# Performance work log

Hardware: AMD Instinct MI355X
Metric: run time of the kernel (lower is better)

The kernel has to match this reference:

```python
import jax, jax.numpy as jnp
import numpy as np
import math

C = 512
EPS = 1e-5


def _ln(x, g, b):
    m = jnp.mean(x, axis=-1, keepdims=True)
    v = jnp.var(x, axis=-1, keepdims=True)
    return (x - m) * jax.lax.rsqrt(v + EPS) * g + b


def _attn(x, w_qkv, w_out):
    # x: (..., L, C); attention over axis -2 (axial)
    qkv = jnp.einsum('...lc,dc->...ld', x, w_qkv)          # (..., L, 3C)
    qkv = qkv.reshape(*qkv.shape[:-1], C, 3)               # interleaved split as in torch reshape(*shape,3)
    q, k, v = qkv[..., 0], qkv[..., 1], qkv[..., 2]
    scale = 1.0 / math.sqrt(C)
    logits = jnp.einsum('...qc,...kc->...qk', q, k) * scale
    p = jax.nn.softmax(logits, axis=-1)
    ctx = jnp.einsum('...qk,...kc->...qc', p, v)
    return jnp.einsum('...lc,dc->...ld', ctx, w_out)


def setup_inputs() -> dict:
    key = jax.random.key(0)
    ks = jax.random.split(key, 16)
    s = 0.02
    inp = {
        'x': jax.random.normal(ks[0], (8, C, 48, 192), jnp.float32),
        'w_qkv1': jax.random.normal(ks[1], (3 * C, C), jnp.float32) * s,
        'w_out1': jax.random.normal(ks[2], (C, C), jnp.float32) * s,
        'w_qkv2': jax.random.normal(ks[3], (3 * C, C), jnp.float32) * s,
        'w_out2': jax.random.normal(ks[4], (C, C), jnp.float32) * s,
        'g1': jnp.ones((C,), jnp.float32), 'b1': jnp.zeros((C,), jnp.float32),
        'g2': jnp.ones((C,), jnp.float32), 'b2': jnp.zeros((C,), jnp.float32),
        'g3': jnp.ones((C,), jnp.float32), 'b3': jnp.zeros((C,), jnp.float32),
        'w_fc1': jax.random.normal(ks[5], (4 * C, C), jnp.float32) * s,
        'b_fc1': jnp.zeros((4 * C,), jnp.float32),
        'w_fc2': jax.random.normal(ks[6], (C, 4 * C), jnp.float32) * s,
        'b_fc2': jnp.zeros((C,), jnp.float32),
    }
    return inp


def reference(x, w_qkv1, w_out1, w_qkv2, w_out2, g1, b1, g2, b2, g3, b3,
              w_fc1, b_fc1, w_fc2, b_fc2):
    # x: (B, C, H, W) -> (B, W, H, C)
    x = jnp.transpose(x, (0, 3, 2, 1))
    x = x + _attn(_ln(x, g1, b1), w_qkv1, w_out1)          # attention along H
    # (B, W, H, C) -> (B, H, W, C)
    x = jnp.transpose(x, (0, 2, 1, 3))
    x = x + _attn(_ln(x, g2, b2), w_qkv2, w_out2)          # attention along W
    h = _ln(x, g3, b3)
    h = jax.nn.relu(jnp.einsum('bhwc,dc->bhwd', h, w_fc1) + b_fc1)
    x = x + jnp.einsum('bhwd,cd->bhwc', h, w_fc2) + b_fc2
    # (B, H, W, C) -> (B, C, H, W)
    return jnp.transpose(x, (0, 3, 1, 2))
```

## Files before the change

### kernel.cpp

```cpp
#include <hip/hip_runtime.h>

typedef unsigned short u16;
typedef __attribute__((ext_vector_type(8))) short short8;
typedef __attribute__((ext_vector_type(8))) __bf16 bf16x8;
typedef __attribute__((ext_vector_type(4))) float f32x4;

#define DEV __device__ __forceinline__

DEV u16 f2bf(float f){ unsigned u = __float_as_uint(f); return (u16)((u + 0x7fffu + ((u>>16)&1u)) >> 16); }
DEV float bf2f(u16 h){ return __uint_as_float(((unsigned)h)<<16); }

DEV f32x4 mfma_bf16(short8 a, short8 b, f32x4 c){
  return __builtin_amdgcn_mfma_f32_16x16x32_bf16(
      __builtin_bit_cast(bf16x8, a), __builtin_bit_cast(bf16x8, b), c, 0, 0, 0);
}

DEV void gl2lds16(const u16* g, u16* s){
  __builtin_amdgcn_global_load_lds(
      (__attribute__((address_space(1))) void*)(g),
      (__attribute__((address_space(3))) void*)(s), 16, 0, 0);
}

#define BB 8
#define HH 48
#define WW 192
#define CC 512
#define NTOK (BB*HH*WW)

__global__ void k_permqkv(const float* __restrict__ w, u16* __restrict__ o){
  int i = blockIdx.x*256 + threadIdx.x;
  int n = i >> 9, kk = i & 511;
  int src = 3*(n & 511) + (n >> 9);
  o[i] = f2bf(w[src*512 + kk]);
}
__global__ void k_conv(const float* __restrict__ w, u16* __restrict__ o, int nelem){
  int i = blockIdx.x*256 + threadIdx.x;
  if (i < nelem) o[i] = f2bf(w[i]);
}

__global__ void k_tin(const float* __restrict__ x, float* __restrict__ xr){
  __shared__ float T[32][33];
  int bh = blockIdx.x / 96, rem = blockIdx.x % 96;
  int c0 = (rem/6)*32, w0 = (rem%6)*32;
  int b = bh / HH, h = bh % HH;
  const float* xp = x + ((size_t)b*CC*HH + h)*WW;
  #pragma unroll
  for (int p=0;p<4;p++){
    int idx = p*256 + threadIdx.x;
    int cc = idx >> 5, ww = idx & 31;
    T[cc][ww] = xp[(size_t)(c0+cc)*(HH*WW) + w0 + ww];
  }
  __syncthreads();
  float* xo = xr + (size_t)bh*WW*CC;
  #pragma unroll
  for (int p=0;p<4;p++){
    int idx = p*256 + threadIdx.x;
    int ww = idx >> 5, cc = idx & 31;
    xo[(size_t)(w0+ww)*CC + c0 + cc] = T[cc][ww];
  }
}

__global__ void k_tout(const float* __restrict__ xr, float* __restrict__ out){
  __shared__ float T[32][33];
  int bh = blockIdx.x / 96, rem = blockIdx.x % 96;
  int c0 = (rem/6)*32, w0 = (rem%6)*32;
  int b = bh / HH, h = bh % HH;
  const float* xi = xr + (size_t)bh*WW*CC;
  #pragma unroll
  for (int p=0;p<4;p++){
    int idx = p*256 + threadIdx.x;
    int ww = idx >> 5, cc = idx & 31;
    T[ww][cc] = xi[(size_t)(w0+ww)*CC + c0 + cc];
  }
  __syncthreads();
  float* op = out + ((size_t)b*CC*HH + h)*WW;
  #pragma unroll
  for (int p=0;p<4;p++){
    int idx = p*256 + threadIdx.x;
    int cc = idx >> 5, ww = idx & 31;
    op[(size_t)(c0+cc)*(HH*WW) + w0 + ww] = T[ww][cc];
  }
}

__global__ void k_ln(const float* __restrict__ xr, const float* __restrict__ g,
                     const float* __restrict__ bb, u16* __restrict__ y){
  int t = blockIdx.x*4 + (threadIdx.x>>6);
  int lane = threadIdx.x & 63;
  const float* row = xr + (size_t)t*CC + lane*8;
  float v[8];
  *(f32x4*)(v)   = *(const f32x4*)(row);
  *(f32x4*)(v+4) = *(const f32x4*)(row+4);
  float s=0.f, s2=0.f;
  #pragma unroll
  for (int j=0;j<8;j++){ s += v[j]; s2 += v[j]*v[j]; }
  #pragma unroll
  for (int o=32;o;o>>=1){ s += __shfl_xor(s,o); s2 += __shfl_xor(s2,o); }
  float mean = s*(1.f/CC);
  float var  = s2*(1.f/CC) - mean*mean;
  float rs = rsqrtf(var + 1e-5f);
  const float* gp = g + lane*8; const float* bp = bb + lane*8;
  short8 o8;
  #pragma unroll
  for (int j=0;j<8;j++) o8[j] = (short)f2bf((v[j]-mean)*rs*gp[j] + bp[j]);
  *(short8*)(y + (size_t)t*CC + lane*8) = o8;
}

__global__ __launch_bounds__(256)
void k_gemm(const u16* __restrict__ A, int lda,
            const u16* __restrict__ Bw, int ldb,
            void* __restrict__ Out, int ldo,
            const float* __restrict__ bias,
            int K, int nbn, int epi){
  __shared__ __align__(16) u16 As[128*64];
  __shared__ __align__(16) u16 Bs[128*64];
  int cpx = gridDim.x >> 3;
  int l = (blockIdx.x & 7)*cpx + (blockIdx.x >> 3);
  int mb = l / nbn, nb = l % nbn;
  int tid = threadIdx.x, lane = tid & 63, wv = tid >> 6;
  size_t m0 = (size_t)mb*128, n0 = (size_t)nb*128;
  int lr = lane >> 3;
  int cc0 = (lane & 7) ^ lr;
  const u16* gA = A  + (m0 + wv*32 + lr)*(size_t)lda + cc0*8;
  const u16* gB = Bw + (n0 + wv*32 + lr)*(size_t)ldb + cc0*8;
  u16* sA = As + wv*32*64;
  u16* sB = Bs + wv*32*64;
  int m = lane & 15, quad = lane >> 4;
  int wm = (wv>>1)*64, wn = (wv&1)*64;
  int off0 = ((quad    ) ^ (m & 7))*8;
  int off1 = ((quad + 4) ^ (m & 7))*8;
  f32x4 acc[4][4];
  #pragma unroll
  for (int i=0;i<4;i++)
    #pragma unroll
    for (int j=0;j<4;j++) acc[i][j] = (f32x4){0.f,0.f,0.f,0.f};
  const u16* aB = As + (wm + m)*64;
  const u16* bB = Bs + (wn + m)*64;
  for (int k0 = 0; k0 < K; k0 += 64){
    #pragma unroll
    for (int t=0;t<4;t++){
      gl2lds16(gA + (size_t)(t*8)*lda, sA + t*8*64);
      gl2lds16(gB + (size_t)(t*8)*ldb, sB + t*8*64);
    }
    gA += 64; gB += 64;
    __syncthreads();
    {
      short8 af[4], bf[4];
      #pragma unroll
      for (int i=0;i<4;i++) af[i] = *(const short8*)(aB + i*16*64 + off0);
      #pragma unroll
      for (int j=0;j<4;j++) bf[j] = *(const short8*)(bB + j*16*64 + off0);
      #pragma unroll
      for (int i=0;i<4;i++)
        #pragma unroll
        for (int j=0;j<4;j++)
          acc[i][j] = mfma_bf16(af[i], bf[j], acc[i][j]);
    }
    {
      short8 af[4], bf[4];
      #pragma unroll
      for (int i=0;i<4;i++) af[i] = *(const short8*)(aB + i*16*64 + off1);
      #pragma unroll
      for (int j=0;j<4;j++) bf[j] = *(const short8*)(bB + j*16*64 + off1);
      #pragma unroll
      for (int i=0;i<4;i++)
        #pragma unroll
        for (int j=0;j<4;j++)
          acc[i][j] = mfma_bf16(af[i], bf[j], acc[i][j]);
    }
    __syncthreads();
  }
  if (epi == 2){
    float* O = (float*)Out + (m0 + wm + quad*4)*(size_t)ldo + n0 + wn + m;
    #pragma unroll
    for (int j=0;j<4;j++){
      float bv = bias ? bias[n0 + wn + j*16 + m] : 0.f;
      #pragma unroll
      for (int i=0;i<4;i++)
        #pragma unroll
        for (int r=0;r<4;r++)
          O[(size_t)(i*16+r)*ldo + j*16] += acc[i][j][r] + bv;
    }
  } else {
    u16* O = (u16*)Out + (m0 + wm + quad*4)*(size_t)ldo + n0 + wn + m;
    #pragma unroll
    for (int j=0;j<4;j++){
      float bv = bias ? bias[n0 + wn + j*16 + m] : 0.f;
      #pragma unroll
      for (int i=0;i<4;i++)
        #pragma unroll
        for (int r=0;r<4;r++){
          float v = acc[i][j][r] + bv;
          if (epi == 1) v = fmaxf(v, 0.f);
          O[(size_t)(i*16+r)*ldo + j*16] = f2bf(v);
        }
    }
  }
}

__global__ void k_qk(const u16* __restrict__ q, const u16* __restrict__ kp, int ldq,
                     float* __restrict__ S, int L, int nt,
                     int SD, int OUTs, int INN, int LST, float scale){
  int blk = blockIdx.x;
  int s = blk / (nt*nt), tl = blk % (nt*nt);
  int ti = tl / nt, tj = tl % nt;
  int lane = threadIdx.x, m = lane & 15, quad = lane >> 4;
  size_t tokbase = (size_t)(s/SD)*OUTs + (size_t)(s%SD)*INN;
  const u16* qr = q  + (tokbase + (size_t)(ti*16+m)*LST)*ldq + quad*8;
  const u16* kr = kp + (tokbase + (size_t)(tj*16+m)*LST)*ldq + quad*8;
  f32x4 acc = (f32x4){0.f,0.f,0.f,0.f};
  #pragma unroll
  for (int kk=0; kk<CC; kk+=32)
    acc = mfma_bf16(*(const short8*)(qr+kk), *(const short8*)(kr+kk), acc);
  float* Sp = S + (size_t)s*L*L + (size_t)(ti*16 + quad*4)*L + tj*16 + m;
  #pragma unroll
  for (int r=0;r<4;r++) Sp[(size_t)r*L] = acc[r]*scale;
}

__global__ void k_softmax(const float* __restrict__ S, u16* __restrict__ P, int L, int Lp){
  int row = blockIdx.x*4 + (threadIdx.x>>6);
  int lane = threadIdx.x & 63;
  const float* sr = S + (size_t)row*L;
  float v0 = (lane      < L) ? sr[lane]      : -3.0e38f;
  float v1 = (lane+64   < L) ? sr[lane+64]   : -3.0e38f;
  float v2 = (lane+128  < L) ? sr[lane+128]  : -3.0e38f;
  float mx = fmaxf(v0, fmaxf(v1, v2));
  #pragma unroll
  for (int o=32;o;o>>=1) mx = fmaxf(mx, __shfl_xor(mx, o));
  float e0 = (lane      < L) ? __expf(v0-mx) : 0.f;
  float e1 = (lane+64   < L) ? __expf(v1-mx) : 0.f;
  float e2 = (lane+128  < L) ? __expf(v2-mx) : 0.f;
  float sm = e0+e1+e2;
  #pragma unroll
  for (int o=32;o;o>>=1) sm += __shfl_xor(sm, o);
  float inv = 1.f/sm;
  u16* pr = P + (size_t)row*Lp;
  if (lane      < Lp) pr[lane]      = f2bf(e0*inv);
  if (lane+64   < Lp) pr[lane+64]   = f2bf(e1*inv);
  if (lane+128  < Lp) pr[lane+128]  = f2bf(e2*inv);
}

__global__ void k_vt(const u16* __restrict__ v, int ldv, u16* __restrict__ vt,
                     int L, int Lp, int SD, int OUTs, int INN, int LST){
  __shared__ float T[32*193];
  int s = blockIdx.x >> 4;
  int c0 = (blockIdx.x & 15)*32;
  size_t tokbase = (size_t)(s/SD)*OUTs + (size_t)(s%SD)*INN;
  int pad = Lp + 1;
  for (int idx = threadIdx.x; idx < L*32; idx += 256){
    int l = idx >> 5, cc = idx & 31;
    T[cc*pad + l] = bf2f(v[(tokbase + (size_t)l*LST)*ldv + c0 + cc]);
  }
  __syncthreads();
  u16* vo = vt + ((size_t)s*CC + c0)*Lp;
  for (int idx = threadIdx.x; idx < 32*Lp; idx += 256){
    int cc = idx / Lp, l = idx - cc*Lp;
    vo[idx] = (l < L) ? f2bf(T[cc*pad + l]) : (u16)0;
  }
}

template<int L, int Lp, int NTQ, int NCJ>
__global__ __launch_bounds__(256)
void k_pv2(const u16* __restrict__ P, const u16* __restrict__ vt, u16* __restrict__ ctx,
           int SD, int OUTs, int INN, int LST){
  constexpr int G   = 32 / NCJ;
  constexpr int LPP = Lp + 8;
  constexpr int CW  = NCJ * 16;
  constexpr int CJW = NCJ / 4;
  constexpr int NKS = Lp / 32;
  constexpr int SHW = (L*LPP > L*CW) ? L*LPP : L*CW;
  __shared__ __align__(16) u16 SH[SHW];

  int sq = blockIdx.x / G, g = blockIdx.x % G;
  int tid = threadIdx.x, lane = tid & 63, wv = tid >> 6;
  int m = lane & 15, quad = lane >> 4;

  const u16* Pg = P + (size_t)sq * L * Lp;
  constexpr int PU = L * Lp / 8;
  for (int u = tid; u < PU; u += 256){
    int r = u / (Lp/8), c = u % (Lp/8);
    *(short8*)(SH + r*LPP + c*8) = *(const short8*)(Pg + (size_t)r*Lp + c*8);
  }
  __syncthreads();

  short8 bfr[CJW][NKS];
  #pragma unroll
  for (int lc = 0; lc < CJW; lc++){
    const u16* vr = vt + ((size_t)sq*CC + (size_t)((g*NCJ + (wv*CJW + lc))*16 + m))*Lp + quad*8;
    #pragma unroll
    for (int ks = 0; ks < NKS; ks++) bfr[lc][ks] = *(const short8*)(vr + ks*32);
  }

  f32x4 acc[CJW][NTQ];
  #pragma unroll
  for (int lc = 0; lc < CJW; lc++)
    #pragma unroll
    for (int qt = 0; qt < NTQ; qt++) acc[lc][qt] = (f32x4){0.f,0.f,0.f,0.f};

  #pragma unroll
  for (int qt = 0; qt < NTQ; qt++){
    short8 a[NKS];
    #pragma unroll
    for (int ks = 0; ks < NKS; ks++)
      a[ks] = *(const short8*)(SH + (qt*16 + m)*LPP + quad*8 + ks*32);
    #pragma unroll
    for (int lc = 0; lc < CJW; lc++)
      #pragma unroll
      for (int ks = 0; ks < NKS; ks++)
        acc[lc][qt] = mfma_bf16(a[ks], bfr[lc][ks], acc[lc][qt]);
  }
  __syncthreads();

  #pragma unroll
  for (int qt = 0; qt < NTQ; qt++)
    #pragma unroll
    for (int lc = 0; lc < CJW; lc++)
      #pragma unroll
      for (int r = 0; r < 4; r++)
        SH[(qt*16 + quad*4 + r)*CW + (wv*CJW + lc)*16 + m] = f2bf(acc[lc][qt][r]);
  __syncthreads();

  size_t tokbase = (size_t)(sq/SD)*OUTs + (size_t)(sq%SD)*INN;
  constexpr int CU8 = CW / 8;
  constexpr int TU = L * CU8;
  for (int u = tid; u < TU; u += 256){
    int l = u / CU8, c = u % CU8;
    *(short8*)(ctx + (tokbase + (size_t)l*LST)*CC + g*CW + c*8) =
        *(const short8*)(SH + l*CW + c*8);
  }
}

extern "C" void kernel_launch(void* const* d_in, const int* in_sizes, int n_in,
                              void* d_out, int out_size, void* d_ws, size_t ws_size,
                              hipStream_t stream){
  const float* x      = (const float*)d_in[0];
  const float* wqkv1  = (const float*)d_in[1];
  const float* wout1  = (const float*)d_in[2];
  const float* wqkv2  = (const float*)d_in[3];
  const float* wout2  = (const float*)d_in[4];
  const float* g1 = (const float*)d_in[5];  const float* b1 = (const float*)d_in[6];
  const float* g2 = (const float*)d_in[7];  const float* b2 = (const float*)d_in[8];
  const float* g3 = (const float*)d_in[9];  const float* b3 = (const float*)d_in[10];
  const float* wfc1 = (const float*)d_in[11]; const float* bfc1 = (const float*)d_in[12];
  const float* wfc2 = (const float*)d_in[13]; const float* bfc2 = (const float*)d_in[14];

  char* ws = (char*)d_ws;
  size_t off = 0;
  auto alloc = [&](size_t bytes)->char*{
    char* p = ws + off; off += (bytes + 255) & ~(size_t)255; return p;
  };
  float* xres = (float*)alloc((size_t)NTOK*CC*4);
  u16*   y    = (u16*)  alloc((size_t)NTOK*CC*2);
  u16*   qkv  = (u16*)  alloc((size_t)NTOK*1536*2);
  u16* wqkv1p = (u16*)alloc((size_t)1536*512*2);
  u16* wqkv2p = (u16*)alloc((size_t)1536*512*2);
  u16* wout1p = (u16*)alloc((size_t)512*512*2);
  u16* wout2p = (u16*)alloc((size_t)512*512*2);
  u16* wfc1p  = (u16*)alloc((size_t)2048*512*2);
  u16* wfc2p  = (u16*)alloc((size_t)512*2048*2);
  u16*   hv   = qkv;

  u16*   P    = (u16*)d_out;
  u16*   vt   = (u16*)((char*)d_out + 28311552);
  float* S    = (float*)((char*)d_out + 28311552);
  (void)ws_size; (void)in_sizes; (void)n_in; (void)out_size;

  const float scale = 0.044194173824159216f;

  k_permqkv<<<3072, 256, 0, stream>>>(wqkv1, wqkv1p);
  k_permqkv<<<3072, 256, 0, stream>>>(wqkv2, wqkv2p);
  k_conv<<<1024, 256, 0, stream>>>(wout1, wout1p, 512*512);
  k_conv<<<1024, 256, 0, stream>>>(wout2, wout2p, 512*512);
  k_conv<<<4096, 256, 0, stream>>>(wfc1, wfc1p, 2048*512);
  k_conv<<<4096, 256, 0, stream>>>(wfc2, wfc2p, 512*2048);

  k_tin<<<BB*HH*96, 256, 0, stream>>>(x, xres);

  k_ln<<<NTOK/4, 256, 0, stream>>>(xres, g1, b1, y);
  k_gemm<<<576*12, 256, 0, stream>>>(y, 512, wqkv1p, 512, qkv, 1536, nullptr, 512, 12, 0);
  k_qk<<<1536*9, 64, 0, stream>>>(qkv, qkv+512, 1536, S, 48, 3, 192, 9216, 1, 192, scale);
  k_softmax<<<NTOK/4, 256, 0, stream>>>(S, P, 48, 64);
  k_vt<<<1536*16, 256, 0, stream>>>(qkv+1024, 1536, vt, 48, 64, 192, 9216, 1, 192);
  k_pv2<48,64,3,16><<<1536*2, 256, 0, stream>>>(P, vt, y, 192, 9216, 1, 192);
  k_gemm<<<576*4, 256, 0, stream>>>(y, 512, wout1p, 512, xres, 512, nullptr, 512, 4, 2);

  k_ln<<<NTOK/4, 256, 0, stream>>>(xres, g2, b2, y);
  k_gemm<<<576*12, 256, 0, stream>>>(y, 512, wqkv2p, 512, qkv, 1536, nullptr, 512, 12, 0);
  k_qk<<<384*144, 64, 0, stream>>>(qkv, qkv+512, 1536, S, 192, 12, 48, 9216, 192, 1, scale);
  k_softmax<<<NTOK/4, 256, 0, stream>>>(S, P, 192, 192);
  k_vt<<<384*16, 256, 0, stream>>>(qkv+1024, 1536, vt, 192, 192, 48, 9216, 192, 1);
  k_pv2<192,192,12,8><<<384*4, 256, 0, stream>>>(P, vt, y, 48, 9216, 192, 1);
  k_gemm<<<576*4, 256, 0, stream>>>(y, 512, wout2p, 512, xres, 512, nullptr, 512, 4, 2);

  k_ln<<<NTOK/4, 256, 0, stream>>>(xres, g3, b3, y);
  for (int half = 0; half < 2; half++){
    size_t M0 = (size_t)half * 36864;
    k_gemm<<<288*16, 256, 0, stream>>>(y + M0*512, 512, wfc1p, 512, hv, 2048, bfc1, 512, 16, 1);
    k_gemm<<<288*4, 256, 0, stream>>>(hv, 2048, wfc2p, 2048, xres + M0*512, 512, bfc2, 2048, 4, 2);
  }

  k_tout<<<BB*HH*96, 256, 0, stream>>>(xres, (float*)d_out);
}
```

Measured before the change: 2.198 ms.

## Rewrite QK^T kernel to stage K tiles in LDS and reuse Q fragments

Replaces the per-16x16-tile QK kernel, which reloaded Q and K rows from global memory for every output tile, with a blocked kernel. Each block keeps a strip of Q rows in registers and streams K in chunks into swizzled LDS via global_load_lds, then computes several output tiles per wave. It also remaps block indices across 8 groups to spread sequences across XCDs. The aim is to cut redundant global traffic and launch overhead, at the cost of larger register use (16 short8 Q fragments) and LDS staging with syncs.

Result: faster. 2.009 ms (-8.6%).

```diff
diff --git a/kernel.cpp b/kernel.cpp
--- a/kernel.cpp
+++ b/kernel.cpp
@@ -197,23 +197,59 @@
   }
 }
 
-__global__ void k_qk(const u16* __restrict__ q, const u16* __restrict__ kp, int ldq,
-                     float* __restrict__ S, int L, int nt,
-                     int SD, int OUTs, int INN, int LST, float scale){
-  int blk = blockIdx.x;
-  int s = blk / (nt*nt), tl = blk % (nt*nt);
-  int ti = tl / nt, tj = tl % nt;
-  int lane = threadIdx.x, m = lane & 15, quad = lane >> 4;
+template<int L, int RPB, int KCH, int NW>
+__global__ __launch_bounds__(64*NW)
+void k_qk2(const u16* __restrict__ q, const u16* __restrict__ kp, int ldq,
+           float* __restrict__ S, int SD, int OUTs, int INN, int LST, float scale){
+  constexpr int NSTRIP = L / RPB;
+  constexpr int NCH = L / KCH;
+  constexpr int RPW = KCH / NW;
+  constexpr int NJT = KCH / 16;
+  __shared__ __align__(16) u16 Ks[KCH*512];
+  int cpx = gridDim.x >> 3;
+  int bl = (blockIdx.x & 7)*cpx + (blockIdx.x >> 3);
+  int s = bl / NSTRIP, st = bl % NSTRIP;
+  int lane = threadIdx.x & 63, wv = threadIdx.x >> 6;
+  int m = lane & 15, quad = lane >> 4;
   size_t tokbase = (size_t)(s/SD)*OUTs + (size_t)(s%SD)*INN;
-  const u16* qr = q  + (tokbase + (size_t)(ti*16+m)*LST)*ldq + quad*8;
-  const u16* kr = kp + (tokbase + (size_t)(tj*16+m)*LST)*ldq + quad*8;
-  f32x4 acc = (f32x4){0.f,0.f,0.f,0.f};
-  #pragma unroll
-  for (int kk=0; kk<CC; kk+=32)
-    acc = mfma_bf16(*(const short8*)(qr+kk), *(const short8*)(kr+kk), acc);
-  float* Sp = S + (size_t)s*L*L + (size_t)(ti*16 + quad*4)*L + tj*16 + m;
-  #pragma unroll
-  for (int r=0;r<4;r++) Sp[(size_t)r*L] = acc[r]*scale;
+
+  const u16* qr = q + (tokbase + (size_t)(st*RPB + wv*16 + m)*LST)*ldq + quad*8;
+  short8 qf[16];
+  #pragma unroll
+  for (int kk=0;kk<16;kk++) qf[kk] = *(const short8*)(qr + kk*32);
+
+  float* Sp = S + (size_t)s*L*L + (size_t)(st*RPB + wv*16 + quad*4)*L;
+
+  for (int ch = 0; ch < NCH; ch++){
+    #pragma unroll
+    for (int rr = 0; rr < RPW; rr++){
+      int row = wv*RPW + rr;
+      gl2lds16(kp + (tokbase + (size_t)(ch*KCH + row)*LST)*ldq + (lane ^ (row & 7))*8,
+               Ks + row*512);
+    }
+    asm volatile("s_waitcnt vmcnt(0)" ::: "memory");
+    __syncthreads();
+
+    f32x4 acc[NJT];
+    #pragma unroll
+    for (int jt=0;jt<NJT;jt++) acc[jt] = (f32x4){0.f,0.f,0.f,0.f};
+    const u16* kB = Ks + m*512;
+    #pragma unroll
+    for (int kk=0;kk<16;kk++){
+      int chunk = ((quad + kk*4) ^ (m & 7))*8;
+      #pragma unroll
+      for (int jt=0;jt<NJT;jt++){
+        short8 bf = *(const short8*)(kB + jt*16*512 + chunk);
+        acc[jt] = mfma_bf16(qf[kk], bf, acc[jt]);
+      }
+    }
+    #pragma unroll
+    for (int jt=0;jt<NJT;jt++)
+      #pragma unroll
+      for (int r=0;r<4;r++)
+        Sp[(size_t)r*L + ch*KCH + jt*16 + m] = acc[jt][r]*scale;
+    if (ch + 1 < NCH) __syncthreads();
+  }
 }
 
 __global__ void k_softmax(const float* __restrict__ S, u16* __restrict__ P, int L, int Lp){
@@ -377,7 +413,7 @@
 
   k_ln<<<NTOK/4, 256, 0, stream>>>(xres, g1, b1, y);
   k_gemm<<<576*12, 256, 0, stream>>>(y, 512, wqkv1p, 512, qkv, 1536, nullptr, 512, 12, 0);
-  k_qk<<<1536*9, 64, 0, stream>>>(qkv, qkv+512, 1536, S, 48, 3, 192, 9216, 1, 192, scale);
+  k_qk2<48,48,48,3><<<1536, 192, 0, stream>>>(qkv, qkv+512, 1536, S, 192, 9216, 1, 192, scale);
   k_softmax<<<NTOK/4, 256, 0, stream>>>(S, P, 48, 64);
   k_vt<<<1536*16, 256, 0, stream>>>(qkv+1024, 1536, vt, 48, 64, 192, 9216, 1, 192);
   k_pv2<48,64,3,16><<<1536*2, 256, 0, stream>>>(P, vt, y, 192, 9216, 1, 192);
@@ -385,7 +421,7 @@
 
   k_ln<<<NTOK/4, 256, 0, stream>>>(xres, g2, b2, y);
   k_gemm<<<576*12, 256, 0, stream>>>(y, 512, wqkv2p, 512, qkv, 1536, nullptr, 512, 12, 0);
-  k_qk<<<384*144, 64, 0, stream>>>(qkv, qkv+512, 1536, S, 192, 12, 48, 9216, 192, 1, scale);
+  k_qk2<192,64,64,4><<<1152, 256, 0, stream>>>(qkv, qkv+512, 1536, S, 48, 9216, 192, 1, scale);
   k_softmax<<<NTOK/4, 256, 0, stream>>>(S, P, 192, 192);
   k_vt<<<384*16, 256, 0, stream>>>(qkv+1024, 1536, vt, 192, 192, 48, 9216, 192, 1);
   k_pv2<192,192,12,8><<<384*4, 256, 0, stream>>>(P, vt, y, 48, 9216, 192, 1);
```
